# Optimization experiments

Measured on AMD Instinct MI355X. Metric: run time of the kernel, lower is better.

## Reference

```python
import jax, jax.numpy as jnp
import numpy as np

DIM = 1024
NUM_HEADS = 16
HEAD_DIM = DIM // NUM_HEADS


def setup_inputs() -> dict:
    key = jax.random.key(0)
    ks = jax.random.split(key, 16)
    B, Sx, Sy = 4, 1024, 1024
    s = 1.0 / np.sqrt(DIM)
    inp = {
        'x': jax.random.normal(ks[0], (B, Sx, DIM), dtype=jnp.float32),
        'y': jax.random.normal(ks[1], (B, Sy, DIM), dtype=jnp.float32),
    }
    names = ['Kx', 'Qx', 'Vx', 'Ky', 'Vy', 'out']
    for i, n in enumerate(names):
        inp[f'W_{n}'] = jax.random.uniform(ks[2 + 2 * i], (DIM, DIM), dtype=jnp.float32, minval=-s, maxval=s)
        inp[f'b_{n}'] = jax.random.uniform(ks[3 + 2 * i], (DIM,), dtype=jnp.float32, minval=-s, maxval=s)
    return inp


def _heads(t, B, S):
    # [B, S, DIM] -> [B, H, S, Dh]
    return t.reshape(B, S, NUM_HEADS, HEAD_DIM).transpose(0, 2, 1, 3)


def _attn(x, y, W_Kx, b_Kx, W_Qx, b_Qx, W_Vx, b_Vx, W_Ky, b_Ky, W_Vy, b_Vy, W_out, b_out):
    B, Sx, _ = x.shape
    Sy = y.shape[1]
    lin = lambda t, W, b: t @ W.T + b
    Q = _heads(lin(x, W_Qx, b_Qx), B, Sx)
    Kc = jnp.concatenate([_heads(lin(x, W_Kx, b_Kx), B, Sx), _heads(lin(y, W_Ky, b_Ky), B, Sy)], axis=2)
    Vc = jnp.concatenate([_heads(lin(x, W_Vx, b_Vx), B, Sx), _heads(lin(y, W_Vy, b_Vy), B, Sy)], axis=2)
    scores = jnp.einsum('bhqd,bhkd->bhqk', Q, Kc) / np.sqrt(HEAD_DIM).astype(np.float32)
    w = jax.nn.softmax(scores, axis=-1)
    o = jnp.einsum('bhqk,bhkd->bhqd', w, Vc)  # [B, H, Sx, Dh]
    o = o.transpose(0, 2, 1, 3).reshape(B, Sx, DIM)
    return lin(o, W_out, b_out)


def reference(x, y, W_Kx, b_Kx, W_Qx, b_Qx, W_Vx, b_Vx, W_Ky, b_Ky, W_Vy, b_Vy, W_out, b_out):
    return _attn(x, y, W_Kx, b_Kx, W_Qx, b_Qx, W_Vx, b_Vx, W_Ky, b_Ky, W_Vy, b_Vy, W_out, b_out)
```

## Files before the change

### kernel.cpp

```cpp
#include <hip/hip_runtime.h>

#define DIMN 1024
#define NH 16
#define DH 64
#define SXX 1024
#define SKV 2048

typedef __bf16 bf16x8 __attribute__((ext_vector_type(8)));
typedef float f32x4 __attribute__((ext_vector_type(4)));
typedef unsigned short us8 __attribute__((ext_vector_type(8)));

__device__ __forceinline__ unsigned short f2bs(float f) {
    return (unsigned short)((__builtin_bit_cast(unsigned int, f) + 0x8000u) >> 16);
}
__device__ __forceinline__ unsigned int pk2(float a, float b) {
    return ((__builtin_bit_cast(unsigned int, a) + 0x8000u) >> 16)
         | ((__builtin_bit_cast(unsigned int, b) + 0x8000u) & 0xffff0000u);
}

struct CvtArgs {
    const float* src[8];
    unsigned short* dst[8];
    int start[8];
};
__global__ __launch_bounds__(256) void cvt_all(CvtArgs a) {
    int b = blockIdx.x;
    int r = 0;
#pragma unroll
    for (int i = 1; i < 8; i++) r += (b >= a.start[i]);
    int off = ((b - a.start[r]) * 256 + (int)threadIdx.x) * 8;
    const float* s = a.src[r] + off;
    float4 f0 = *(const float4*)(s);
    float4 f1 = *(const float4*)(s + 4);
    us8 o;
    o[0] = f2bs(f0.x); o[1] = f2bs(f0.y); o[2] = f2bs(f0.z); o[3] = f2bs(f0.w);
    o[4] = f2bs(f1.x); o[5] = f2bs(f1.y); o[6] = f2bs(f1.z); o[7] = f2bs(f1.w);
    *(us8*)(a.dst[r] + off) = o;
}

__device__ __forceinline__ void gemm_core(const unsigned short* __restrict__ A,
                                          const unsigned short* __restrict__ W,
                                          unsigned short* As, unsigned short* Bs,
                                          int m0, int n0, f32x4 (&acc)[4][4]) {
    const int K = DIMN;
    int tid = threadIdx.x, wave = tid >> 6, lane = tid & 63;
    int l15 = lane & 15, quad = lane >> 4;
    int wm = wave >> 1, wn = wave & 1;
    int srow = wave * 8 + (lane >> 3);
    int gcol = ((lane & 7) ^ (lane >> 3)) * 8;
    const unsigned short* gA = A + (size_t)(m0 + srow) * K + gcol;
    const unsigned short* gW = W + (size_t)(n0 + srow) * K + gcol;
    int ldswr = wave * 512 + lane * 8;
    int slot0 = (quad ^ (l15 & 7)) * 8;

    us8 pa[4], pw[4];
    auto gload = [&](int k0) {
#pragma unroll
        for (int j = 0; j < 4; j++) {
            pa[j] = *(const us8*)(gA + k0 + (size_t)j * 32 * K);
            pw[j] = *(const us8*)(gW + k0 + (size_t)j * 32 * K);
        }
    };
    auto lwrite = [&]() {
#pragma unroll
        for (int j = 0; j < 4; j++) {
            *(us8*)(&As[ldswr + j * 2048]) = pa[j];
            *(us8*)(&Bs[ldswr + j * 2048]) = pw[j];
        }
    };

    gload(0);
    for (int k0 = 0; k0 < K; k0 += 64) {
        if (k0) __syncthreads();
        lwrite();
        if (k0 + 64 < K) gload(k0 + 64);
        __syncthreads();
#pragma unroll
        for (int kk = 0; kk < 2; kk++) {
            int sl = slot0 ^ (kk * 32);
            bf16x8 af[4], bf[4];
#pragma unroll
            for (int mi = 0; mi < 4; mi++)
                af[mi] = __builtin_bit_cast(bf16x8, *(const us8*)(&As[(wm * 64 + mi * 16 + l15) * 64 + sl]));
#pragma unroll
            for (int ni = 0; ni < 4; ni++)
                bf[ni] = __builtin_bit_cast(bf16x8, *(const us8*)(&Bs[(wn * 64 + ni * 16 + l15) * 64 + sl]));
#pragma unroll
            for (int mi = 0; mi < 4; mi++)
#pragma unroll
                for (int ni = 0; ni < 4; ni++)
                    acc[mi][ni] = __builtin_amdgcn_mfma_f32_16x16x32_bf16(af[mi], bf[ni], acc[mi][ni], 0, 0, 0);
        }
    }
}

__global__ __launch_bounds__(256, 2) void gemm_proj(
        const unsigned short* __restrict__ xb, const unsigned short* __restrict__ yb,
        const unsigned short* __restrict__ Wb,
        const float* __restrict__ b_Kx, const float* __restrict__ b_Qx, const float* __restrict__ b_Ky,
        const float* __restrict__ b_Vx, const float* __restrict__ b_Vy,
        unsigned short* __restrict__ Qd, unsigned short* __restrict__ Kd,
        unsigned short* __restrict__ Vd, float qscale) {
    __shared__ __align__(16) unsigned short As[128 * 64];
    __shared__ __align__(16) unsigned short Bs[128 * 64];
    int bx = blockIdx.x;
    int tid = threadIdx.x, wave = tid >> 6, lane = tid & 63;
    int l15 = lane & 15, quad = lane >> 4;
    int wm = wave >> 1, wn = wave & 1;

    f32x4 acc[4][4] = {};

    if (bx < 768) {
        int sub = bx >> 8, t = bx & 255;
        int n0 = (t & 7) * 128, m0 = (t >> 3) * 128;
        const unsigned short* A = (sub == 2) ? yb : xb;
        const unsigned short* W = Wb + (size_t)((sub == 0) ? 0 : (sub == 1) ? 1 : 3) * 1048576;
        const float* bp = (sub == 0) ? b_Kx : (sub == 1) ? b_Qx : b_Ky;
        int roff = (sub == 2) ? 1024 : 0;
        float sc = (sub == 1) ? qscale : 1.0f;

        gemm_core(A, W, As, Bs, m0, n0, acc);

#pragma unroll
        for (int mi = 0; mi < 4; mi++) {
            int mbase = m0 + wm * 64 + mi * 16 + quad * 4;
#pragma unroll
            for (int ni = 0; ni < 4; ni++) {
                int n = n0 + wn * 64 + ni * 16 + l15;
                float bv = bp[n];
                int h = n >> 6, d = n & 63;
#pragma unroll
                for (int r = 0; r < 4; r++) {
                    float v = (acc[mi][ni][r] + bv) * sc;
                    int mm = mbase + r;
                    int bidx = mm >> 10, s = mm & 1023;
                    if (sub == 1)
                        Qd[((size_t)(bidx * NH + h) * SXX + s) * DH + d] = f2bs(v);
                    else
                        Kd[((size_t)(bidx * NH + h) * SKV + s + roff) * DH + d] = f2bs(v);
                }
            }
        }
    } else {
        int u = bx - 768;
        int side = u >> 8, t = u & 255;
        int m0 = (t & 7) * 128, n0 = (t >> 3) * 128;
        const unsigned short* Wv = Wb + (size_t)(side ? 4 : 2) * 1048576;
        const unsigned short* act = side ? yb : xb;
        const float* bp = side ? b_Vy : b_Vx;
        int roff = side ? 1024 : 0;

        gemm_core(Wv, act, As, Bs, m0, n0, acc);

#pragma unroll
        for (int mi = 0; mi < 4; mi++) {
            int mbase = m0 + wm * 64 + mi * 16 + quad * 4;
#pragma unroll
            for (int ni = 0; ni < 4; ni++) {
                int n = n0 + wn * 64 + ni * 16 + l15;
                int bidx = n >> 10, s = n & 1023;
#pragma unroll
                for (int r = 0; r < 4; r++) {
                    int m = mbase + r;
                    int h = m >> 6, d = m & 63;
                    float v = acc[mi][ni][r] + bp[m];
                    Vd[((size_t)(bidx * NH + h) * DH + d) * SKV + s + roff] = f2bs(v);
                }
            }
        }
    }
}

__global__ __launch_bounds__(256, 2) void gemm_out(
        const unsigned short* __restrict__ Ob, const unsigned short* __restrict__ Wo,
        const float* __restrict__ bo, float* __restrict__ outp) {
    __shared__ __align__(16) unsigned short As[64 * 64];
    __shared__ __align__(16) unsigned short Bs[128 * 64];
    const int K = DIMN;
    int tid = threadIdx.x, wave = tid >> 6, lane = tid & 63;
    int l15 = lane & 15, quad = lane >> 4;
    int wm = wave >> 1, wn = wave & 1;
    int n0 = blockIdx.x * 128, m0 = blockIdx.y * 64;

    int srow = wave * 8 + (lane >> 3);
    int gcol = ((lane & 7) ^ (lane >> 3)) * 8;
    const unsigned short* gA = Ob + (size_t)(m0 + srow) * K + gcol;
    const unsigned short* gW = Wo + (size_t)(n0 + srow) * K + gcol;
    int ldswr = wave * 512 + lane * 8;
    int slot0 = (quad ^ (l15 & 7)) * 8;

    us8 pa[2], pw[4];
    auto gload = [&](int k0) {
#pragma unroll
        for (int j = 0; j < 2; j++)
            pa[j] = *(const us8*)(gA + k0 + (size_t)j * 32 * K);
#pragma unroll
        for (int j = 0; j < 4; j++)
            pw[j] = *(const us8*)(gW + k0 + (size_t)j * 32 * K);
    };
    auto lwrite = [&]() {
#pragma unroll
        for (int j = 0; j < 2; j++)
            *(us8*)(&As[ldswr + j * 2048]) = pa[j];
#pragma unroll
        for (int j = 0; j < 4; j++)
            *(us8*)(&Bs[ldswr + j * 2048]) = pw[j];
    };

    f32x4 acc[2][4] = {};
    gload(0);
    for (int k0 = 0; k0 < K; k0 += 64) {
        if (k0) __syncthreads();
        lwrite();
        if (k0 + 64 < K) gload(k0 + 64);
        __syncthreads();
#pragma unroll
        for (int kk = 0; kk < 2; kk++) {
            int sl = slot0 ^ (kk * 32);
            bf16x8 af[2], bf[4];
#pragma unroll
            for (int mi = 0; mi < 2; mi++)
                af[mi] = __builtin_bit_cast(bf16x8, *(const us8*)(&As[(wm * 32 + mi * 16 + l15) * 64 + sl]));
#pragma unroll
            for (int ni = 0; ni < 4; ni++)
                bf[ni] = __builtin_bit_cast(bf16x8, *(const us8*)(&Bs[(wn * 64 + ni * 16 + l15) * 64 + sl]));
#pragma unroll
            for (int mi = 0; mi < 2; mi++)
#pragma unroll
                for (int ni = 0; ni < 4; ni++)
                    acc[mi][ni] = __builtin_amdgcn_mfma_f32_16x16x32_bf16(af[mi], bf[ni], acc[mi][ni], 0, 0, 0);
        }
    }

#pragma unroll
    for (int mi = 0; mi < 2; mi++) {
        int mbase = m0 + wm * 32 + mi * 16 + quad * 4;
#pragma unroll
        for (int ni = 0; ni < 4; ni++) {
            int n = n0 + wn * 64 + ni * 16 + l15;
            float bv = bo[n];
#pragma unroll
            for (int r = 0; r < 4; r++)
                outp[(size_t)(mbase + r) * DIMN + n] = acc[mi][ni][r] + bv;
        }
    }
}

__global__ __launch_bounds__(256, 2) void flash_attn(
        const unsigned short* __restrict__ Qb,
        const unsigned short* __restrict__ Kc,
        const unsigned short* __restrict__ Vt,
        unsigned short* __restrict__ Ob) {
    __shared__ __align__(16) unsigned short Ks[2][64 * 64];
    __shared__ __align__(16) unsigned short Vs[2][64 * 64];
    __shared__ __align__(16) unsigned short Ps[4][32 * 64];
    int tid = threadIdx.x, wave = tid >> 6, lane = tid & 63;
    int l15 = lane & 15, quad = lane >> 4;
    int bh = blockIdx.x;
    int qbase = blockIdx.y * 128 + wave * 32;

    const unsigned short* Qp = Qb + ((size_t)bh * SXX + qbase) * DH;
    bf16x8 bq[2][2];
#pragma unroll
    for (int qt = 0; qt < 2; qt++) {
        bq[qt][0] = __builtin_bit_cast(bf16x8, *(const us8*)(&Qp[(qt * 16 + l15) * DH + quad * 8]));
        bq[qt][1] = __builtin_bit_cast(bf16x8, *(const us8*)(&Qp[(qt * 16 + l15) * DH + 32 + quad * 8]));
    }

    const unsigned short* Kg = Kc + (size_t)bh * SKV * DH;
    const unsigned short* Vg = Vt + (size_t)bh * DH * SKV;

    int srow_lo = 8 * wave + (lane >> 3);
    int srow_hi = srow_lo + 32;
    int swz = ((lane & 7) ^ (lane >> 3)) * 8;
    int sl = (lane & 7) * 8;

    us8 pk0, pk1, pv0, pv1;
    auto gload = [&](int c) {
        pk0 = *(const us8*)(Kg + (size_t)(c + srow_lo) * DH + swz);
        pk1 = *(const us8*)(Kg + (size_t)(c + srow_hi) * DH + swz);
        pv0 = *(const us8*)(Vg + (size_t)srow_lo * SKV + c + swz);
        pv1 = *(const us8*)(Vg + (size_t)srow_hi * SKV + c + swz);
    };
    auto lstore = [&](int buf) {
        *(us8*)(&Ks[buf][srow_lo * 64 + sl]) = pk0;
        *(us8*)(&Ks[buf][srow_hi * 64 + sl]) = pk1;
        *(us8*)(&Vs[buf][srow_lo * 64 + sl]) = pv0;
        *(us8*)(&Vs[buf][srow_hi * 64 + sl]) = pv1;
    };

    f32x4 o[2][4] = {};
    float lsum[2] = {0.f, 0.f};
    int cA = (quad ^ (l15 & 7)) * 8;

    gload(0);
    lstore(0);
    __syncthreads();

    for (int c = 0; c < SKV; c += 64) {
        int cur = (c >> 6) & 1;
        bool more = (c + 64) < SKV;
        if (more) gload(c + 64);

        const unsigned short* ks = &Ks[cur][0];
        bf16x8 ak0[4], ak1[4];
#pragma unroll
        for (int ni = 0; ni < 4; ni++) {
            int row = (ni * 16 + l15) * 64;
            ak0[ni] = __builtin_bit_cast(bf16x8, *(const us8*)(ks + row + cA));
            ak1[ni] = __builtin_bit_cast(bf16x8, *(const us8*)(ks + row + (cA ^ 32)));
        }

        unsigned short* pw = &Ps[wave][0];
#pragma unroll
        for (int qt = 0; qt < 2; qt++) {
#pragma unroll
            for (int ni = 0; ni < 4; ni++) {
                f32x4 z = {};
                z = __builtin_amdgcn_mfma_f32_16x16x32_bf16(ak0[ni], bq[qt][0], z, 0, 0, 0);
                z = __builtin_amdgcn_mfma_f32_16x16x32_bf16(ak1[ni], bq[qt][1], z, 0, 0, 0);
                float p0 = __builtin_amdgcn_exp2f(z[0]);
                float p1 = __builtin_amdgcn_exp2f(z[1]);
                float p2 = __builtin_amdgcn_exp2f(z[2]);
                float p3 = __builtin_amdgcn_exp2f(z[3]);
                lsum[qt] += (p0 + p1) + (p2 + p3);
                unsigned int lo = pk2(p0, p1);
                unsigned int hi = pk2(p2, p3);
                int c8p = (2 * ni + (quad >> 1)) ^ (l15 & 7);
                *(uint2*)(pw + (qt * 16 + l15) * 64 + c8p * 8 + (quad & 1) * 4) = make_uint2(lo, hi);
            }
        }

        const unsigned short* vs = &Vs[cur][0];
        bf16x8 av0[4], av1[4];
#pragma unroll
        for (int ni = 0; ni < 4; ni++) {
            int row = (ni * 16 + l15) * 64;
            av0[ni] = __builtin_bit_cast(bf16x8, *(const us8*)(vs + row + cA));
            av1[ni] = __builtin_bit_cast(bf16x8, *(const us8*)(vs + row + (cA ^ 32)));
        }
#pragma unroll
        for (int qt = 0; qt < 2; qt++) {
            bf16x8 ap0 = __builtin_bit_cast(bf16x8, *(const us8*)(pw + (qt * 16 + l15) * 64 + cA));
            bf16x8 ap1 = __builtin_bit_cast(bf16x8, *(const us8*)(pw + (qt * 16 + l15) * 64 + (cA ^ 32)));
#pragma unroll
            for (int ni = 0; ni < 4; ni++) {
                o[qt][ni] = __builtin_amdgcn_mfma_f32_16x16x32_bf16(ap0, av0[ni], o[qt][ni], 0, 0, 0);
                o[qt][ni] = __builtin_amdgcn_mfma_f32_16x16x32_bf16(ap1, av1[ni], o[qt][ni], 0, 0, 0);
            }
        }

        if (more) lstore(1 - cur);
        __syncthreads();
    }

    int b = bh >> 4, h = bh & 15;
#pragma unroll
    for (int qt = 0; qt < 2; qt++) {
        float ls = lsum[qt];
        ls += __shfl_xor(ls, 16);
        ls += __shfl_xor(ls, 32);
#pragma unroll
        for (int r = 0; r < 4; r++) {
            float lt = __shfl(ls, quad * 4 + r);
            float inv = __builtin_amdgcn_rcpf(lt);
            int q = qbase + qt * 16 + quad * 4 + r;
#pragma unroll
            for (int ni = 0; ni < 4; ni++)
                Ob[((size_t)b * SXX + q) * DIMN + h * DH + ni * 16 + l15] = f2bs(o[qt][ni][r] * inv);
        }
    }
}

extern "C" void kernel_launch(void* const* d_in, const int* in_sizes, int n_in,
                              void* d_out, int out_size, void* d_ws, size_t ws_size,
                              hipStream_t stream) {
    (void)in_sizes; (void)n_in; (void)out_size; (void)ws_size;
    const float* x     = (const float*)d_in[0];
    const float* y     = (const float*)d_in[1];
    const float* W_Kx  = (const float*)d_in[2];
    const float* b_Kx  = (const float*)d_in[3];
    const float* W_Qx  = (const float*)d_in[4];
    const float* b_Qx  = (const float*)d_in[5];
    const float* W_Vx  = (const float*)d_in[6];
    const float* b_Vx  = (const float*)d_in[7];
    const float* W_Ky  = (const float*)d_in[8];
    const float* b_Ky  = (const float*)d_in[9];
    const float* W_Vy  = (const float*)d_in[10];
    const float* b_Vy  = (const float*)d_in[11];
    const float* W_out = (const float*)d_in[12];
    const float* b_out = (const float*)d_in[13];
    float* out = (float*)d_out;

    char* ws = (char*)d_ws;
    unsigned short* xb  = (unsigned short*)(ws);
    unsigned short* yb  = (unsigned short*)(ws + (size_t)( 8 << 20));
    unsigned short* Qb  = (unsigned short*)(ws + (size_t)(16 << 20));
    unsigned short* Kcw = (unsigned short*)(ws + (size_t)(24 << 20));
    unsigned short* Vtw = (unsigned short*)(ws + (size_t)(40 << 20));
    unsigned short* Obw = (unsigned short*)(ws + (size_t)(56 << 20));
    unsigned short* Wb  = (unsigned short*)(ws + (size_t)(64 << 20));

    CvtArgs ca;
    ca.src[0] = x;     ca.dst[0] = xb;                 ca.start[0] = 0;
    ca.src[1] = y;     ca.dst[1] = yb;                 ca.start[1] = 2048;
    ca.src[2] = W_Kx;  ca.dst[2] = Wb + 0u * 1048576;  ca.start[2] = 4096;
    ca.src[3] = W_Qx;  ca.dst[3] = Wb + 1u * 1048576;  ca.start[3] = 4608;
    ca.src[4] = W_Vx;  ca.dst[4] = Wb + 2u * 1048576;  ca.start[4] = 5120;
    ca.src[5] = W_Ky;  ca.dst[5] = Wb + 3u * 1048576;  ca.start[5] = 5632;
    ca.src[6] = W_Vy;  ca.dst[6] = Wb + 4u * 1048576;  ca.start[6] = 6144;
    ca.src[7] = W_out; ca.dst[7] = Wb + 5u * 1048576;  ca.start[7] = 6656;
    cvt_all<<<7168, 256, 0, stream>>>(ca);

    const float qscale = 0.125f * 1.44269504088896340736f;
    gemm_proj<<<1280, 256, 0, stream>>>(xb, yb, Wb, b_Kx, b_Qx, b_Ky, b_Vx, b_Vy,
                                        Qb, Kcw, Vtw, qscale);
    flash_attn<<<dim3(64, 8), 256, 0, stream>>>(Qb, Kcw, Vtw, Obw);
    gemm_out<<<dim3(8, 64), 256, 0, stream>>>(Obw, Wb + 5u * 1048576, b_out, out);
}
```

Before: 236.0 us.

## Keep attention probabilities in registers and feed 16x16x16 MFMA directly

Drops the per-wave LDS round trip for the softmax probabilities in flash attention. The S accumulator layout is reused directly as the A operand of the 16x16x16 bf16 MFMA, and V fragments are read in a matching swizzled layout. This removes LDS writes and reads of P and frees shared memory, at the cost of twice as many smaller MFMA instructions. Occupancy hints for the two GEMM kernels are also raised from 2 to 3 blocks per CU, which may limit registers.

```diff
diff --git a/kernel.cpp b/kernel.cpp
--- a/kernel.cpp
+++ b/kernel.cpp
@@ -9,6 +9,8 @@
 typedef __bf16 bf16x8 __attribute__((ext_vector_type(8)));
 typedef float f32x4 __attribute__((ext_vector_type(4)));
 typedef unsigned short us8 __attribute__((ext_vector_type(8)));
+typedef short s16x4 __attribute__((ext_vector_type(4)));
+typedef unsigned int u32x2 __attribute__((ext_vector_type(2)));
 
 __device__ __forceinline__ unsigned short f2bs(float f) {
     return (unsigned short)((__builtin_bit_cast(unsigned int, f) + 0x8000u) >> 16);
@@ -94,7 +96,7 @@
     }
 }
 
-__global__ __launch_bounds__(256, 2) void gemm_proj(
+__global__ __launch_bounds__(256, 3) void gemm_proj(
         const unsigned short* __restrict__ xb, const unsigned short* __restrict__ yb,
         const unsigned short* __restrict__ Wb,
         const float* __restrict__ b_Kx, const float* __restrict__ b_Qx, const float* __restrict__ b_Ky,
@@ -171,7 +173,7 @@
     }
 }
 
-__global__ __launch_bounds__(256, 2) void gemm_out(
+__global__ __launch_bounds__(256, 3) void gemm_out(
         const unsigned short* __restrict__ Ob, const unsigned short* __restrict__ Wo,
         const float* __restrict__ bo, float* __restrict__ outp) {
     __shared__ __align__(16) unsigned short As[64 * 64];
@@ -253,7 +255,6 @@
         unsigned short* __restrict__ Ob) {
     __shared__ __align__(16) unsigned short Ks[2][64 * 64];
     __shared__ __align__(16) unsigned short Vs[2][64 * 64];
-    __shared__ __align__(16) unsigned short Ps[4][32 * 64];
     int tid = threadIdx.x, wave = tid >> 6, lane = tid & 63;
     int l15 = lane & 15, quad = lane >> 4;
     int bh = blockIdx.x;
@@ -311,44 +312,42 @@
             ak1[ni] = __builtin_bit_cast(bf16x8, *(const us8*)(ks + row + (cA ^ 32)));
         }
 
-        unsigned short* pw = &Ps[wave][0];
+        s16x4 af[2][4];
 #pragma unroll
         for (int qt = 0; qt < 2; qt++) {
 #pragma unroll
-            for (int ni = 0; ni < 4; ni++) {
+            for (int t = 0; t < 4; t++) {
                 f32x4 z = {};
-                z = __builtin_amdgcn_mfma_f32_16x16x32_bf16(ak0[ni], bq[qt][0], z, 0, 0, 0);
-                z = __builtin_amdgcn_mfma_f32_16x16x32_bf16(ak1[ni], bq[qt][1], z, 0, 0, 0);
+                z = __builtin_amdgcn_mfma_f32_16x16x32_bf16(ak0[t], bq[qt][0], z, 0, 0, 0);
+                z = __builtin_amdgcn_mfma_f32_16x16x32_bf16(ak1[t], bq[qt][1], z, 0, 0, 0);
                 float p0 = __builtin_amdgcn_exp2f(z[0]);
                 float p1 = __builtin_amdgcn_exp2f(z[1]);
                 float p2 = __builtin_amdgcn_exp2f(z[2]);
                 float p3 = __builtin_amdgcn_exp2f(z[3]);
                 lsum[qt] += (p0 + p1) + (p2 + p3);
-                unsigned int lo = pk2(p0, p1);
-                unsigned int hi = pk2(p2, p3);
-                int c8p = (2 * ni + (quad >> 1)) ^ (l15 & 7);
-                *(uint2*)(pw + (qt * 16 + l15) * 64 + c8p * 8 + (quad & 1) * 4) = make_uint2(lo, hi);
+                u32x2 u; u[0] = pk2(p0, p1); u[1] = pk2(p2, p3);
+                af[qt][t] = __builtin_bit_cast(s16x4, u);
             }
         }
 
         const unsigned short* vs = &Vs[cur][0];
-        bf16x8 av0[4], av1[4];
-#pragma unroll
-        for (int ni = 0; ni < 4; ni++) {
-            int row = (ni * 16 + l15) * 64;
-            av0[ni] = __builtin_bit_cast(bf16x8, *(const us8*)(vs + row + cA));
-            av1[ni] = __builtin_bit_cast(bf16x8, *(const us8*)(vs + row + (cA ^ 32)));
-        }
-#pragma unroll
-        for (int qt = 0; qt < 2; qt++) {
-            bf16x8 ap0 = __builtin_bit_cast(bf16x8, *(const us8*)(pw + (qt * 16 + l15) * 64 + cA));
-            bf16x8 ap1 = __builtin_bit_cast(bf16x8, *(const us8*)(pw + (qt * 16 + l15) * 64 + (cA ^ 32)));
-#pragma unroll
-            for (int ni = 0; ni < 4; ni++) {
-                o[qt][ni] = __builtin_amdgcn_mfma_f32_16x16x32_bf16(ap0, av0[ni], o[qt][ni], 0, 0, 0);
-                o[qt][ni] = __builtin_amdgcn_mfma_f32_16x16x32_bf16(ap1, av1[ni], o[qt][ni], 0, 0, 0);
+        s16x4 vf[4][4];
+#pragma unroll
+        for (int nd = 0; nd < 4; nd++) {
+            int drow = (nd * 16 + l15) * 64;
+#pragma unroll
+            for (int t = 0; t < 4; t++) {
+                int slt = ((2 * t + (quad >> 1)) ^ (l15 & 7)) * 8 + (quad & 1) * 4;
+                vf[nd][t] = *(const s16x4*)(vs + drow + slt);
             }
         }
+#pragma unroll
+        for (int qt = 0; qt < 2; qt++)
+#pragma unroll
+            for (int nd = 0; nd < 4; nd++)
+#pragma unroll
+                for (int t = 0; t < 4; t++)
+                    o[qt][nd] = __builtin_amdgcn_mfma_f32_16x16x16bf16_1k(af[qt][t], vf[nd][t], o[qt][nd], 0, 0, 0);
 
         if (more) lstore(1 - cur);
         __syncthreads();
```

Result: slower. 244.4 us (+3.6%).

## Load V fragments directly from global into registers, drop V LDS staging

Applied to the files above, without the earlier changes.

The flash attention kernel no longer stages V tiles through shared memory. Each wave reads its MFMA B-operand fragments of transposed V straight from global memory every iteration. The P buffer swizzle gains an extra XOR term to reduce bank conflicts. This cuts LDS capacity and LDS write/read traffic for V, but every wave now re-reads V from global/L2 without a prefetch stage, which may expose load latency. The two GEMM kernels also raise their launch-bounds occupancy hint from 2 to 3.

```diff
diff --git a/kernel.cpp b/kernel.cpp
--- a/kernel.cpp
+++ b/kernel.cpp
@@ -94,7 +94,7 @@
     }
 }
 
-__global__ __launch_bounds__(256, 2) void gemm_proj(
+__global__ __launch_bounds__(256, 3) void gemm_proj(
         const unsigned short* __restrict__ xb, const unsigned short* __restrict__ yb,
         const unsigned short* __restrict__ Wb,
         const float* __restrict__ b_Kx, const float* __restrict__ b_Qx, const float* __restrict__ b_Ky,
@@ -171,7 +171,7 @@
     }
 }
 
-__global__ __launch_bounds__(256, 2) void gemm_out(
+__global__ __launch_bounds__(256, 3) void gemm_out(
         const unsigned short* __restrict__ Ob, const unsigned short* __restrict__ Wo,
         const float* __restrict__ bo, float* __restrict__ outp) {
     __shared__ __align__(16) unsigned short As[64 * 64];
@@ -252,7 +252,6 @@
         const unsigned short* __restrict__ Vt,
         unsigned short* __restrict__ Ob) {
     __shared__ __align__(16) unsigned short Ks[2][64 * 64];
-    __shared__ __align__(16) unsigned short Vs[2][64 * 64];
     __shared__ __align__(16) unsigned short Ps[4][32 * 64];
     int tid = threadIdx.x, wave = tid >> 6, lane = tid & 63;
     int l15 = lane & 15, quad = lane >> 4;
@@ -275,32 +274,38 @@
     int swz = ((lane & 7) ^ (lane >> 3)) * 8;
     int sl = (lane & 7) * 8;
 
-    us8 pk0, pk1, pv0, pv1;
-    auto gload = [&](int c) {
+    us8 pk0, pk1;
+    auto gloadK = [&](int c) {
         pk0 = *(const us8*)(Kg + (size_t)(c + srow_lo) * DH + swz);
         pk1 = *(const us8*)(Kg + (size_t)(c + srow_hi) * DH + swz);
-        pv0 = *(const us8*)(Vg + (size_t)srow_lo * SKV + c + swz);
-        pv1 = *(const us8*)(Vg + (size_t)srow_hi * SKV + c + swz);
-    };
-    auto lstore = [&](int buf) {
+    };
+    auto lstoreK = [&](int buf) {
         *(us8*)(&Ks[buf][srow_lo * 64 + sl]) = pk0;
         *(us8*)(&Ks[buf][srow_hi * 64 + sl]) = pk1;
-        *(us8*)(&Vs[buf][srow_lo * 64 + sl]) = pv0;
-        *(us8*)(&Vs[buf][srow_hi * 64 + sl]) = pv1;
     };
 
     f32x4 o[2][4] = {};
     float lsum[2] = {0.f, 0.f};
     int cA = (quad ^ (l15 & 7)) * 8;
-
-    gload(0);
-    lstore(0);
+    int hx = (l15 >> 3) << 2;
+    int cAP = ((quad ^ (l15 & 7)) ^ hx) * 8;
+    const unsigned short* vbase = Vg + (size_t)l15 * SKV + quad * 8;
+
+    gloadK(0);
+    lstoreK(0);
     __syncthreads();
 
     for (int c = 0; c < SKV; c += 64) {
         int cur = (c >> 6) & 1;
         bool more = (c + 64) < SKV;
-        if (more) gload(c + 64);
+        if (more) gloadK(c + 64);
+
+        us8 vf0[4], vf1[4];
+#pragma unroll
+        for (int nd = 0; nd < 4; nd++) {
+            vf0[nd] = *(const us8*)(vbase + (size_t)(nd * 16) * SKV + c);
+            vf1[nd] = *(const us8*)(vbase + (size_t)(nd * 16) * SKV + c + 32);
+        }
 
         const unsigned short* ks = &Ks[cur][0];
         bf16x8 ak0[4], ak1[4];
@@ -326,31 +331,23 @@
                 lsum[qt] += (p0 + p1) + (p2 + p3);
                 unsigned int lo = pk2(p0, p1);
                 unsigned int hi = pk2(p2, p3);
-                int c8p = (2 * ni + (quad >> 1)) ^ (l15 & 7);
+                int c8p = ((2 * ni + (quad >> 1)) ^ (l15 & 7)) ^ hx;
                 *(uint2*)(pw + (qt * 16 + l15) * 64 + c8p * 8 + (quad & 1) * 4) = make_uint2(lo, hi);
             }
         }
 
-        const unsigned short* vs = &Vs[cur][0];
-        bf16x8 av0[4], av1[4];
-#pragma unroll
-        for (int ni = 0; ni < 4; ni++) {
-            int row = (ni * 16 + l15) * 64;
-            av0[ni] = __builtin_bit_cast(bf16x8, *(const us8*)(vs + row + cA));
-            av1[ni] = __builtin_bit_cast(bf16x8, *(const us8*)(vs + row + (cA ^ 32)));
-        }
 #pragma unroll
         for (int qt = 0; qt < 2; qt++) {
-            bf16x8 ap0 = __builtin_bit_cast(bf16x8, *(const us8*)(pw + (qt * 16 + l15) * 64 + cA));
-            bf16x8 ap1 = __builtin_bit_cast(bf16x8, *(const us8*)(pw + (qt * 16 + l15) * 64 + (cA ^ 32)));
-#pragma unroll
-            for (int ni = 0; ni < 4; ni++) {
-                o[qt][ni] = __builtin_amdgcn_mfma_f32_16x16x32_bf16(ap0, av0[ni], o[qt][ni], 0, 0, 0);
-                o[qt][ni] = __builtin_amdgcn_mfma_f32_16x16x32_bf16(ap1, av1[ni], o[qt][ni], 0, 0, 0);
+            bf16x8 ap0 = __builtin_bit_cast(bf16x8, *(const us8*)(pw + (qt * 16 + l15) * 64 + cAP));
+            bf16x8 ap1 = __builtin_bit_cast(bf16x8, *(const us8*)(pw + (qt * 16 + l15) * 64 + (cAP ^ 32)));
+#pragma unroll
+            for (int nd = 0; nd < 4; nd++) {
+                o[qt][nd] = __builtin_amdgcn_mfma_f32_16x16x32_bf16(ap0, __builtin_bit_cast(bf16x8, vf0[nd]), o[qt][nd], 0, 0, 0);
+                o[qt][nd] = __builtin_amdgcn_mfma_f32_16x16x32_bf16(ap1, __builtin_bit_cast(bf16x8, vf1[nd]), o[qt][nd], 0, 0, 0);
             }
         }
 
-        if (more) lstore(1 - cur);
+        if (more) lstoreK(1 - cur);
         __syncthreads();
     }
 
```

Result: slower. 260.4 us (+10.3%).
